# Performance work log

Measured on AMD Instinct MI355X. Metric: run time of the kernel, lower is better.

## Reference

```python
import jax, jax.numpy as jnp
import numpy as np

H, W, P, Q, K_STEP = 32, 32, 12, 12, 12
NUM_CELLS = H * W
TE_DEPTH = 24 * 7  # 168
# 8 neighbor directions: positions 0..8 of a 3x3 stencil, excluding center (4)
DIRS = [(r, c) for r in range(3) for c in range(3) if not (r == 1 and c == 1)]


def setup_inputs() -> dict:
    key = jax.random.key(0)
    k1, k2, k3, k4, k5, k6 = jax.random.split(key, 6)
    B = 4
    X = jax.random.uniform(k1, (B, P, H, W, 1), dtype=jnp.float32)
    day = jax.random.randint(k2, (B, P + Q, 1), 0, 7, dtype=jnp.int32)
    hour = jax.random.randint(k3, (B, P + Q, 1), 0, 24, dtype=jnp.int32)
    TE = jnp.concatenate([day, hour], axis=-1)  # [B, P+Q, 2]
    F = TE_DEPTH + NUM_CELLS  # 1192
    s = 1.0 / np.sqrt(F)
    W_trans = jax.random.normal(k4, (F, 8), dtype=jnp.float32) * s
    W_restart = jax.random.normal(k5, (F, 1), dtype=jnp.float32) * s
    W_bias = jax.random.normal(k6, (F, 1), dtype=jnp.float32) * s
    return {"X": X, "TE": TE, "W_trans": W_trans, "W_restart": W_restart, "W_bias": W_bias}


def _te_pos_P(TE, B, dtype):
    # one-hot time encoding [B,T,168] tiled over the grid
    te_idx = TE[..., 0] * 24 + TE[..., 1]
    te_oh = jax.nn.one_hot(te_idx, TE_DEPTH, dtype=dtype)  # [B,T,168]
    te_b = jnp.broadcast_to(te_oh[:, :P, None, None, :], (B, P, H, W, TE_DEPTH))
    # positional one-hot per cell: identity reshaped to [H,W,H*W]
    pos = jnp.eye(NUM_CELLS, dtype=dtype).reshape(H, W, NUM_CELLS)
    pos_b = jnp.broadcast_to(pos[None, None], (B, P, H, W, NUM_CELLS))
    return jnp.concatenate([te_b, pos_b], axis=-1)  # [B,P,H,W,1192]


def reference(X, TE, W_trans, W_restart, W_bias):
    B = X.shape[0]
    TE_pos_P = _te_pos_P(TE, B, X.dtype)
    trans_prob = jax.nn.softmax(TE_pos_P @ W_trans, axis=-1)      # [B,P,H,W,8]
    restart_prob = jax.nn.sigmoid(TE_pos_P @ W_restart)           # [B,P,H,W,1]
    X_bias = (TE_pos_P @ W_bias) * X                              # [B,P,H,W,1]
    x = X
    results = [x]
    for _ in range(K_STEP):
        xn = x * trans_prob                                       # [B,P,H,W,8]
        xn_pad = jnp.pad(xn, ((0, 0), (0, 0), (1, 1), (1, 1), (0, 0)))
        # 8-neighbor shift-gather (equivalent to the one-hot conv3d)
        x_trans = sum(xn_pad[:, :, r:r + H, c:c + W, d] for d, (r, c) in enumerate(DIRS))
        x_trans = x_trans[..., None]                              # [B,P,H,W,1]
        x = (1.0 - restart_prob) * x_trans + restart_prob * x + X_bias
        results.append(x)
    Y = x[:, -1:]
    return (Y, x, trans_prob[..., None], restart_prob, jnp.stack(results, axis=-1))
```

## Files before the change

kernel.cpp:

```cpp
#include <hip/hip_runtime.h>


namespace {
constexpr int PP  = 12;
constexpr int NC  = 1024;
constexpr int TED = 168;
constexpr int KS  = 12;
constexpr int PAD = 34;
constexpr long O_X   = 4096;
constexpr long O_TP  = 53248;
constexpr long O_RP  = 446464;
constexpr long O_RES = 495616;
}

__global__ __launch_bounds__(1024) void rwr_fused(
    const float* __restrict__ X,
    const int* __restrict__ TE,
    const float* __restrict__ Wt,
    const float* __restrict__ Wr,
    const float* __restrict__ Wb,
    float* __restrict__ out)
{
    __shared__ float tp[NC * 8];
    __shared__ float xb0[PAD * PAD];
    __shared__ float xb1[PAD * PAD];

    const int bp   = blockIdx.x;
    const int b    = bp / PP;
    const int p    = bp - b * PP;
    const int cell = threadIdx.x;
    const int h    = cell >> 5;
    const int w    = cell & 31;

    for (int i = threadIdx.x; i < PAD * PAD; i += 1024) { xb0[i] = 0.f; xb1[i] = 0.f; }
    __syncthreads();

    const int te = TE[(b * 24 + p) * 2 + 0] * 24 + TE[(b * 24 + p) * 2 + 1];

    float pr[8];
    float m = -1e30f;
    #pragma unroll
    for (int j = 0; j < 8; ++j) {
        pr[j] = Wt[te * 8 + j] + Wt[(TED + cell) * 8 + j];
        m = fmaxf(m, pr[j]);
    }
    float s = 0.f;
    #pragma unroll
    for (int j = 0; j < 8; ++j) { pr[j] = __expf(pr[j] - m); s += pr[j]; }
    const float inv = 1.f / s;
    #pragma unroll
    for (int j = 0; j < 8; ++j) { pr[j] *= inv; tp[cell * 8 + j] = pr[j]; }

    const float rp    = 1.f / (1.f + __expf(-(Wr[te] + Wr[TED + cell])));
    const float x0    = X[bp * NC + cell];
    const float xbias = (Wb[te] + Wb[TED + cell]) * x0;

    xb0[(h + 1) * PAD + (w + 1)] = x0;
    __syncthreads();

    const int drr[8] = {-1,-1,-1, 0, 0, 1, 1, 1};
    const int dcc[8] = {-1, 0, 1,-1, 1,-1, 0, 1};
    float wn[8];
    #pragma unroll
    for (int d = 0; d < 8; ++d) {
        const int nh = h + drr[d], nw = w + dcc[d];
        const bool ok = ((unsigned)nh < 32u) && ((unsigned)nw < 32u);
        const int nidx = ok ? (nh * 32 + nw) : 0;
        wn[d] = tp[nidx * 8 + d];
    }

    float res[KS + 1];
    res[0] = x0;
    float x = x0;
    float* cur = xb0;
    float* nxt = xb1;
    #pragma unroll
    for (int k = 0; k < KS; ++k) {
        float xt = 0.f;
        #pragma unroll
        for (int d = 0; d < 8; ++d)
            xt += wn[d] * cur[(h + 1 + drr[d]) * PAD + (w + 1 + dcc[d])];
        x = (1.f - rp) * xt + rp * x + xbias;
        res[k + 1] = x;
        nxt[(h + 1) * PAD + (w + 1)] = x;
        float* t = cur; cur = nxt; nxt = t;
        __syncthreads();
    }

    const long gci = (long)bp * NC + cell;
    out[O_X + gci] = x;
    #pragma unroll
    for (int j = 0; j < 8; ++j) out[O_TP + gci * 8 + j] = pr[j];
    out[O_RP + gci] = rp;
    #pragma unroll
    for (int k = 0; k <= KS; ++k) out[O_RES + gci * 13 + k] = res[k];
    if (p == PP - 1) out[(long)b * NC + cell] = x;
}

extern "C" void kernel_launch(void* const* d_in, const int* in_sizes, int n_in,
                              void* d_out, int out_size, void* d_ws, size_t ws_size,
                              hipStream_t stream) {
    const float* X  = (const float*)d_in[0];
    const int*   TE = (const int*)d_in[1];
    const float* Wt = (const float*)d_in[2];
    const float* Wr = (const float*)d_in[3];
    const float* Wb = (const float*)d_in[4];
    float* out = (float*)d_out;

    rwr_fused<<<dim3(4 * PP), dim3(1024), 0, stream>>>(X, TE, Wt, Wr, Wb, out);
}
```

Before: 68.85 us.

## Process four cells per thread with vectorized LDS stencil loads and 256-thread blocks

Each thread now handles four horizontally adjacent cells, so blocks shrink from 1024 to 256 threads. Stencil neighbours are loaded as float4 rows from a padded, aligned shared grid and reused across the four cells. Transition probabilities are stored transposed and padded in shared memory, and the global writes are vectorized. The aim is to cut LDS traffic and the cost of each per-step barrier; the trade-off is fewer threads per block and more registers per thread, with only 48 blocks in the grid.

```diff
diff --git a/kernel.cpp b/kernel.cpp
--- a/kernel.cpp
+++ b/kernel.cpp
@@ -2,18 +2,21 @@
 
 
 namespace {
-constexpr int PP  = 12;
-constexpr int NC  = 1024;
-constexpr int TED = 168;
-constexpr int KS  = 12;
-constexpr int PAD = 34;
+constexpr int PP   = 12;
+constexpr int NC   = 1024;
+constexpr int TED  = 168;
+constexpr int KS   = 12;
+constexpr int PADW = 40;
+constexpr int GSZ  = 34 * PADW;
+constexpr int TPR  = 33;
+constexpr int TPD  = 32 * TPR;
 constexpr long O_X   = 4096;
 constexpr long O_TP  = 53248;
 constexpr long O_RP  = 446464;
 constexpr long O_RES = 495616;
 }
 
-__global__ __launch_bounds__(1024) void rwr_fused(
+__global__ __launch_bounds__(256, 1) void rwr_fused(
     const float* __restrict__ X,
     const int* __restrict__ TE,
     const float* __restrict__ Wt,
@@ -21,80 +24,135 @@
     const float* __restrict__ Wb,
     float* __restrict__ out)
 {
-    __shared__ float tp[NC * 8];
-    __shared__ float xb0[PAD * PAD];
-    __shared__ float xb1[PAD * PAD];
+    __shared__ __align__(16) float tpT[8 * TPD];
+    __shared__ __align__(16) float xg[2 * GSZ];
 
-    const int bp   = blockIdx.x;
-    const int b    = bp / PP;
-    const int p    = bp - b * PP;
-    const int cell = threadIdx.x;
-    const int h    = cell >> 5;
-    const int w    = cell & 31;
+    const int bp    = blockIdx.x;
+    const int bIdx  = bp / PP;
+    const int p     = bp - bIdx * PP;
+    const int t     = threadIdx.x;
+    const int h     = t >> 3;
+    const int w0    = (t & 7) << 2;
+    const int cell0 = (h << 5) + w0;
+    const long gci0 = (long)bp * NC + cell0;
 
-    for (int i = threadIdx.x; i < PAD * PAD; i += 1024) { xb0[i] = 0.f; xb1[i] = 0.f; }
+    {
+        const float4 z4 = make_float4(0.f, 0.f, 0.f, 0.f);
+        float4* xg4 = (float4*)xg;
+        for (int i = t; i < (2 * GSZ) / 4; i += 256) xg4[i] = z4;
+    }
+
+    const int te = TE[(bIdx * 24 + p) * 2 + 0] * 24 + TE[(bIdx * 24 + p) * 2 + 1];
+
+    float teRow[8];
+    #pragma unroll
+    for (int j = 0; j < 8; ++j) teRow[j] = Wt[te * 8 + j];
+
+    float pr[4][8];
+    #pragma unroll
+    for (int c = 0; c < 4; ++c) {
+        const float4 a = *(const float4*)&Wt[(TED + cell0 + c) * 8];
+        const float4 d = *(const float4*)&Wt[(TED + cell0 + c) * 8 + 4];
+        float l[8] = {a.x, a.y, a.z, a.w, d.x, d.y, d.z, d.w};
+        float m = -1e30f;
+        #pragma unroll
+        for (int j = 0; j < 8; ++j) { l[j] += teRow[j]; m = fmaxf(m, l[j]); }
+        float s = 0.f;
+        #pragma unroll
+        for (int j = 0; j < 8; ++j) { l[j] = __expf(l[j] - m); s += l[j]; }
+        const float inv = 1.f / s;
+        #pragma unroll
+        for (int j = 0; j < 8; ++j) pr[c][j] = l[j] * inv;
+    }
+
+    const float4 wr4 = *(const float4*)&Wr[TED + cell0];
+    const float4 wb4 = *(const float4*)&Wb[TED + cell0];
+    const float4 x04 = *(const float4*)&X[(long)bp * NC + cell0];
+    const float  wrTe = Wr[te], wbTe = Wb[te];
+    const float wrArr[4] = {wr4.x, wr4.y, wr4.z, wr4.w};
+    const float wbArr[4] = {wb4.x, wb4.y, wb4.z, wb4.w};
+    const float x0Arr[4] = {x04.x, x04.y, x04.z, x04.w};
+
+    float rp_[4], xb_[4], x_[4];
+    float res[4][13];
+    #pragma unroll
+    for (int c = 0; c < 4; ++c) {
+        rp_[c] = 1.f / (1.f + __expf(-(wrTe + wrArr[c])));
+        xb_[c] = (wbTe + wbArr[c]) * x0Arr[c];
+        x_[c]  = x0Arr[c];
+        res[c][0] = x0Arr[c];
+    }
+
     __syncthreads();
 
-    const int te = TE[(b * 24 + p) * 2 + 0] * 24 + TE[(b * 24 + p) * 2 + 1];
+    #pragma unroll
+    for (int c = 0; c < 4; ++c)
+        #pragma unroll
+        for (int j = 0; j < 8; ++j)
+            tpT[j * TPD + h * TPR + (w0 + c)] = pr[c][j];
+    *(float4*)&xg[(h + 1) * PADW + w0 + 4] = make_float4(x_[0], x_[1], x_[2], x_[3]);
 
-    float pr[8];
-    float m = -1e30f;
     #pragma unroll
-    for (int j = 0; j < 8; ++j) {
-        pr[j] = Wt[te * 8 + j] + Wt[(TED + cell) * 8 + j];
-        m = fmaxf(m, pr[j]);
+    for (int c = 0; c < 4; ++c) {
+        *(float4*)&out[O_TP + (gci0 + c) * 8]     = make_float4(pr[c][0], pr[c][1], pr[c][2], pr[c][3]);
+        *(float4*)&out[O_TP + (gci0 + c) * 8 + 4] = make_float4(pr[c][4], pr[c][5], pr[c][6], pr[c][7]);
     }
-    float s = 0.f;
-    #pragma unroll
-    for (int j = 0; j < 8; ++j) { pr[j] = __expf(pr[j] - m); s += pr[j]; }
-    const float inv = 1.f / s;
-    #pragma unroll
-    for (int j = 0; j < 8; ++j) { pr[j] *= inv; tp[cell * 8 + j] = pr[j]; }
+    *(float4*)&out[O_RP + gci0] = make_float4(rp_[0], rp_[1], rp_[2], rp_[3]);
 
-    const float rp    = 1.f / (1.f + __expf(-(Wr[te] + Wr[TED + cell])));
-    const float x0    = X[bp * NC + cell];
-    const float xbias = (Wb[te] + Wb[TED + cell]) * x0;
-
-    xb0[(h + 1) * PAD + (w + 1)] = x0;
     __syncthreads();
 
     const int drr[8] = {-1,-1,-1, 0, 0, 1, 1, 1};
     const int dcc[8] = {-1, 0, 1,-1, 1,-1, 0, 1};
-    float wn[8];
+    float wn[4][8];
     #pragma unroll
-    for (int d = 0; d < 8; ++d) {
-        const int nh = h + drr[d], nw = w + dcc[d];
-        const bool ok = ((unsigned)nh < 32u) && ((unsigned)nw < 32u);
-        const int nidx = ok ? (nh * 32 + nw) : 0;
-        wn[d] = tp[nidx * 8 + d];
+    for (int c = 0; c < 4; ++c) {
+        const int wc = w0 + c;
+        #pragma unroll
+        for (int d = 0; d < 8; ++d) {
+            const int nh = h + drr[d], nw = wc + dcc[d];
+            const bool ok = ((unsigned)nh < 32u) && ((unsigned)nw < 32u);
+            const int idx = ok ? (d * TPD + nh * TPR + nw) : 0;
+            wn[c][d] = tpT[idx];
+        }
     }
 
-    float res[KS + 1];
-    res[0] = x0;
-    float x = x0;
-    float* cur = xb0;
-    float* nxt = xb1;
+    float* cur = xg;
+    float* nxt = xg + GSZ;
+    const int rA = h * PADW + w0;
+    const int rB = rA + PADW;
+    const int rC = rB + PADW;
     #pragma unroll
     for (int k = 0; k < KS; ++k) {
-        float xt = 0.f;
+        float T[6], M[6], Bt[6];
+        { const float4 v = *(const float4*)&cur[rA + 4];
+          T[0]=cur[rA+3]; T[1]=v.x; T[2]=v.y; T[3]=v.z; T[4]=v.w; T[5]=cur[rA+8]; }
+        { const float4 v = *(const float4*)&cur[rB + 4];
+          M[0]=cur[rB+3]; M[1]=v.x; M[2]=v.y; M[3]=v.z; M[4]=v.w; M[5]=cur[rB+8]; }
+        { const float4 v = *(const float4*)&cur[rC + 4];
+          Bt[0]=cur[rC+3]; Bt[1]=v.x; Bt[2]=v.y; Bt[3]=v.z; Bt[4]=v.w; Bt[5]=cur[rC+8]; }
+
         #pragma unroll
-        for (int d = 0; d < 8; ++d)
-            xt += wn[d] * cur[(h + 1 + drr[d]) * PAD + (w + 1 + dcc[d])];
-        x = (1.f - rp) * xt + rp * x + xbias;
-        res[k + 1] = x;
-        nxt[(h + 1) * PAD + (w + 1)] = x;
-        float* t = cur; cur = nxt; nxt = t;
+        for (int c = 0; c < 4; ++c) {
+            const float xt = wn[c][0]*T[c]  + wn[c][1]*T[c+1]  + wn[c][2]*T[c+2]
+                           + wn[c][3]*M[c]  + wn[c][4]*M[c+2]
+                           + wn[c][5]*Bt[c] + wn[c][6]*Bt[c+1] + wn[c][7]*Bt[c+2];
+            const float xv = (1.f - rp_[c]) * xt + rp_[c] * x_[c] + xb_[c];
+            x_[c] = xv;
+            res[c][k + 1] = xv;
+        }
+        *(float4*)&nxt[rB + 4] = make_float4(x_[0], x_[1], x_[2], x_[3]);
+        { float* tsw = cur; cur = nxt; nxt = tsw; }
         __syncthreads();
     }
 
-    const long gci = (long)bp * NC + cell;
-    out[O_X + gci] = x;
+    *(float4*)&out[O_X + gci0] = make_float4(x_[0], x_[1], x_[2], x_[3]);
     #pragma unroll
-    for (int j = 0; j < 8; ++j) out[O_TP + gci * 8 + j] = pr[j];
-    out[O_RP + gci] = rp;
-    #pragma unroll
-    for (int k = 0; k <= KS; ++k) out[O_RES + gci * 13 + k] = res[k];
-    if (p == PP - 1) out[(long)b * NC + cell] = x;
+    for (int c = 0; c < 4; ++c)
+        #pragma unroll
+        for (int k = 0; k <= KS; ++k)
+            out[O_RES + (gci0 + c) * 13 + k] = res[c][k];
+    if (p == PP - 1)
+        *(float4*)&out[(long)bIdx * NC + cell0] = make_float4(x_[0], x_[1], x_[2], x_[3]);
 }
 
 extern "C" void kernel_launch(void* const* d_in, const int* in_sizes, int n_in,
@@ -107,5 +165,5 @@
     const float* Wb = (const float*)d_in[4];
     float* out = (float*)d_out;
 
-    rwr_fused<<<dim3(4 * PP), dim3(1024), 0, stream>>>(X, TE, Wt, Wr, Wb, out);
+    rwr_fused<<<dim3(4 * PP), dim3(256), 0, stream>>>(X, TE, Wt, Wr, Wb, out);
 }
```

Result: slower. 71.00 us (+3.1%).
